# Optimization experiments

Measured on AMD Instinct MI355X. Metric: run time of the kernel, lower is better.

The kernel has to match this reference:

```python
import jax, jax.numpy as jnp
import numpy as np
from math import sqrt

B, L, S, H, E, D = 2, 2048, 2048, 16, 64, 64

def setup_inputs() -> dict:
    key = jax.random.key(0)
    kq, kk, kv = jax.random.split(key, 3)
    queries = jax.random.normal(kq, (B, L, H, E), dtype=jnp.float32)
    keys = jax.random.normal(kk, (B, S, H, E), dtype=jnp.float32)
    values = jax.random.normal(kv, (B, S, H, D), dtype=jnp.float32)
    # causal mask: True where attention is NOT allowed (j > i), matching masked_fill_ semantics
    causal = jnp.triu(jnp.ones((L, S), dtype=jnp.bool_), k=1)
    attn_mask = jnp.broadcast_to(causal[None, None, :, :], (B, 1, L, S))
    return {"queries": queries, "keys": keys, "values": values, "attn_mask": attn_mask}

def reference(queries, keys, values, attn_mask):
    # scores: [B,H,L,S]
    scale = 1.0 / sqrt(queries.shape[-1])
    scores = jnp.einsum('blhe,bshe->bhls', queries, keys)
    scores = jnp.where(attn_mask, -jnp.inf, scores)
    A = jax.nn.softmax(scale * scores, axis=-1)
    V = jnp.einsum('bhls,bshd->blhd', A, values)
    return V
```

## Files before the change

kernel.cpp:

```cpp
#include <hip/hip_runtime.h>

typedef unsigned short ushort_t;
typedef __attribute__((ext_vector_type(8))) short s8v;
typedef __attribute__((ext_vector_type(4))) short s4v;
typedef __attribute__((ext_vector_type(4))) float f4;

__device__ __forceinline__ ushort_t f2bf(float x) {
    unsigned u = __builtin_bit_cast(unsigned, x);
    return (ushort_t)((u + 0x7FFFu + ((u >> 16) & 1u)) >> 16);
}

__global__ __launch_bounds__(256) void prep_k(const float* __restrict__ K,
                                              ushort_t* __restrict__ Kb) {
    const int gid = blockIdx.x * 256 + threadIdx.x;
    const int e = (gid & 7) * 8;
    const int h = (gid >> 3) & 15;
    const int s = (gid >> 7) & 2047;
    const int b = gid >> 18;
    const float* src = K + (((b * 2048 + s) * 16 + h) * 64 + e);
    f4 a = *(const f4*)src;
    f4 c = *(const f4*)(src + 4);
    s8v o;
    #pragma unroll
    for (int j = 0; j < 4; ++j) { o[j] = (short)f2bf(a[j]); o[j + 4] = (short)f2bf(c[j]); }
    *(s8v*)(Kb + (((b * 16 + h) * 2048 + s) * 64 + e)) = o;
}

__global__ __launch_bounds__(256) void prep_v(const float* __restrict__ V,
                                              ushort_t* __restrict__ VT) {
    __shared__ ushort_t T[64 * 72];
    const int s0 = (blockIdx.x & 31) * 64;
    const int h  = (blockIdx.x >> 5) & 15;
    const int b  = blockIdx.x >> 9;
    const int t  = threadIdx.x;
    {
        const int srow = t >> 2, dc = (t & 3) * 16;
        const float* src = V + (((b * 2048 + s0 + srow) * 16 + h) * 64 + dc);
        #pragma unroll
        for (int c = 0; c < 4; ++c) {
            f4 v = *(const f4*)(src + c * 4);
            #pragma unroll
            for (int j = 0; j < 4; ++j) T[(dc + c * 4 + j) * 72 + srow] = f2bf(v[j]);
        }
    }
    __syncthreads();
    {
        const int d = t >> 2, sq = (t & 3) * 16;
        ushort_t* dst = VT + (((b * 16 + h) * 64 + d) * 2048 + s0 + sq);
        *(s8v*)(dst)     = *(const s8v*)(&T[d * 72 + sq]);
        *(s8v*)(dst + 8) = *(const s8v*)(&T[d * 72 + sq + 8]);
    }
}

__global__ __launch_bounds__(128, 2) void fattn_main(
    const float* __restrict__ Q,
    const ushort_t* __restrict__ Kb,
    const ushort_t* __restrict__ VTb,
    float* __restrict__ O)
{
    constexpr float K1 = 0.18033688011112042f;
    constexpr float SHIFT = 12.0f;
    __shared__ ushort_t P[2][4 * 640];
    __shared__ float Obuf[32 * 64];
    __shared__ float Lbuf[32];

    const int bx = blockIdx.x;
    const int bh = (bx & 7) | (((bx >> 3) & 3) << 3);
    const int pr = bx >> 5;
    const int b = bh >> 4, h = bh & 15;

    const int wave = threadIdx.x >> 6;
    const int lane = threadIdx.x & 63;
    const int l15  = lane & 15;
    const int quad = lane >> 4;

    const ushort_t* kb  = Kb  + bh * (2048 * 64);
    const ushort_t* vtb = VTb + bh * (64 * 2048);
    const float*    qb  = Q + b * (2048 * 1024) + h * 64;
    float*          ob  = O + b * (2048 * 1024) + h * 64;

    const s8v ones = {0x3F80, 0x3F80, 0x3F80, 0x3F80, 0x3F80, 0x3F80, 0x3F80, 0x3F80};
    const f4 zero4 = {0.f, 0.f, 0.f, 0.f};
    ushort_t* Pw = P[wave];

    for (int half = 0; half < 2; ++half) {
        const int i   = half ? (63 - pr) : pr;
        const int qr0 = i * 32;
        const int il  = i >> 1;

        s8v aq[2][2];
        #pragma unroll
        for (int m = 0; m < 2; ++m) {
            const float* qrow = qb + (qr0 + m * 16 + l15) * 1024;
            #pragma unroll
            for (int ks = 0; ks < 2; ++ks) {
                f4 x = *(const f4*)(qrow + ks * 32 + quad * 8);
                f4 y = *(const f4*)(qrow + ks * 32 + quad * 8 + 4);
                #pragma unroll
                for (int j = 0; j < 4; ++j) {
                    aq[m][ks][j]     = (short)f2bf(x[j]);
                    aq[m][ks][j + 4] = (short)f2bf(y[j]);
                }
            }
        }

        f4 oacc[2][4];
        f4 lsum[2] = {zero4, zero4};
        #pragma unroll
        for (int m = 0; m < 2; ++m)
            #pragma unroll
            for (int d = 0; d < 4; ++d) oacc[m][d] = zero4;

        for (int it = wave; it <= il; it += 2) {
            const int n0 = it * 64;
            const ushort_t* kp = kb + n0 * 64;
            const ushort_t* vp = vtb + n0;

            s8v bk[4][2];
            #pragma unroll
            for (int t = 0; t < 4; ++t)
                #pragma unroll
                for (int ks = 0; ks < 2; ++ks)
                    bk[t][ks] = *(const s8v*)(kp + (t * 16 + l15) * 64 + ks * 32 + quad * 8);
            s8v bv[4][2];
            #pragma unroll
            for (int dd = 0; dd < 4; ++dd)
                #pragma unroll
                for (int ks = 0; ks < 2; ++ks)
                    bv[dd][ks] = *(const s8v*)(vp + (dd * 16 + l15) * 2048 + ks * 32 + quad * 8);

            f4 sacc[2][4];
            #pragma unroll
            for (int m = 0; m < 2; ++m)
                #pragma unroll
                for (int t = 0; t < 4; ++t) {
                    f4 a = __builtin_amdgcn_mfma_f32_16x16x32_bf16(aq[m][0], bk[t][0], zero4, 0, 0, 0);
                    sacc[m][t] = __builtin_amdgcn_mfma_f32_16x16x32_bf16(aq[m][1], bk[t][1], a, 0, 0, 0);
                }

            const bool diag = (it == il);
            #pragma unroll
            for (int m = 0; m < 2; ++m)
                #pragma unroll
                for (int t = 0; t < 4; ++t)
                    #pragma unroll
                    for (int r = 0; r < 4; ++r) {
                        float x = __builtin_fmaf(sacc[m][t][r], K1, -SHIFT);
                        if (diag) {
                            const int gi = qr0 + m * 16 + quad * 4 + r;
                            const int gj = n0 + t * 16 + l15;
                            if (gj > gi) x = -INFINITY;
                        }
                        const float p = __builtin_exp2f(x);
                        const unsigned pb = __builtin_bit_cast(unsigned, p);
                        Pw[t * 640 + (m * 16 + quad * 4 + r) * 20 + l15] = (ushort_t)(pb >> 16);
                    }

            #pragma unroll
            for (int m = 0; m < 2; ++m)
                #pragma unroll
                for (int ks = 0; ks < 2; ++ks) {
                    const ushort_t* pp = Pw + (ks * 2 + (quad >> 1)) * 640
                                            + (m * 16 + l15) * 20 + (quad & 1) * 8;
                    s4v p0 = *(const s4v*)(pp);
                    s4v p1 = *(const s4v*)(pp + 4);
                    s8v ap = __builtin_shufflevector(p0, p1, 0, 1, 2, 3, 4, 5, 6, 7);
                    lsum[m] = __builtin_amdgcn_mfma_f32_16x16x32_bf16(ap, ones, lsum[m], 0, 0, 0);
                    #pragma unroll
                    for (int dd = 0; dd < 4; ++dd)
                        oacc[m][dd] = __builtin_amdgcn_mfma_f32_16x16x32_bf16(ap, bv[dd][ks], oacc[m][dd], 0, 0, 0);
                }
        }

        __syncthreads();
        if (wave == 1) {
            #pragma unroll
            for (int m = 0; m < 2; ++m) {
                #pragma unroll
                for (int dd = 0; dd < 4; ++dd)
                    #pragma unroll
                    for (int r = 0; r < 4; ++r)
                        Obuf[(m * 16 + quad * 4 + r) * 64 + dd * 16 + l15] = oacc[m][dd][r];
                if (l15 == 0)
                    #pragma unroll
                    for (int r = 0; r < 4; ++r) Lbuf[m * 16 + quad * 4 + r] = lsum[m][r];
            }
        }
        __syncthreads();
        if (wave == 0) {
            #pragma unroll
            for (int m = 0; m < 2; ++m)
                #pragma unroll
                for (int r = 0; r < 4; ++r) {
                    const int row = m * 16 + quad * 4 + r;
                    const float inv = 1.0f / (lsum[m][r] + Lbuf[row]);
                    #pragma unroll
                    for (int dd = 0; dd < 4; ++dd)
                        ob[(qr0 + row) * 1024 + dd * 16 + l15] =
                            (oacc[m][dd][r] + Obuf[row * 64 + dd * 16 + l15]) * inv;
                }
        }
    }
}

#define PSTR 72
__global__ __launch_bounds__(256) void fattn_fallback(
    const float* __restrict__ Q, const float* __restrict__ K,
    const float* __restrict__ V, float* __restrict__ O)
{
    constexpr int strL = 1024, strB = 2048 * strL;
    const float scale = 0.125f;
    __shared__ ushort_t KT[64 * PSTR];
    __shared__ ushort_t VT[64 * PSTR];
    __shared__ ushort_t P[4][16 * PSTR];
    const int bh = blockIdx.x & 31;
    const int b = bh >> 4, h = bh & 15;
    const int im = 31 - (blockIdx.x >> 5);
    const int q0 = im * 64;
    const int tid = threadIdx.x, wave = tid >> 6, lane = tid & 63;
    const int l15 = lane & 15, quad = lane >> 4;
    const float* qbase = Q + b*strB + (q0 + wave*16 + l15)*strL + h*64;
    s8v aq0, aq1;
    {
        f4 q0v = *(const f4*)(qbase + quad*8);
        f4 q1v = *(const f4*)(qbase + quad*8 + 4);
        f4 q2v = *(const f4*)(qbase + 32 + quad*8);
        f4 q3v = *(const f4*)(qbase + 32 + quad*8 + 4);
        #pragma unroll
        for (int j = 0; j < 4; ++j) {
            aq0[j] = (short)f2bf(q0v[j]); aq0[j+4] = (short)f2bf(q1v[j]);
            aq1[j] = (short)f2bf(q2v[j]); aq1[j+4] = (short)f2bf(q3v[j]);
        }
    }
    const f4 zero4 = {0.f,0.f,0.f,0.f};
    f4 oacc[4]; float m_prev[4], lsum[4];
    #pragma unroll
    for (int d = 0; d < 4; ++d) oacc[d] = zero4;
    #pragma unroll
    for (int r = 0; r < 4; ++r) { m_prev[r] = -INFINITY; lsum[r] = 0.0f; }
    const float* kh = K + b*strB + h*64;
    const float* vh = V + b*strB + h*64;
    for (int it = 0; it <= im; ++it) {
        const int n0 = it * 64;
        __syncthreads();
        {
            const float* krow = kh + (n0 + lane)*strL + wave*16;
            f4 k0 = *(const f4*)(krow); f4 k1 = *(const f4*)(krow+4);
            f4 k2 = *(const f4*)(krow+8); f4 k3 = *(const f4*)(krow+12);
            s8v kb0, kb1;
            #pragma unroll
            for (int j = 0; j < 4; ++j) {
                kb0[j] = (short)f2bf(k0[j]); kb0[j+4] = (short)f2bf(k1[j]);
                kb1[j] = (short)f2bf(k2[j]); kb1[j+4] = (short)f2bf(k3[j]);
            }
            *(s8v*)&KT[lane*PSTR + wave*16] = kb0;
            *(s8v*)&KT[lane*PSTR + wave*16 + 8] = kb1;
            const float* vrow = vh + (n0 + lane)*strL + wave*16;
            f4 v0 = *(const f4*)(vrow); f4 v1 = *(const f4*)(vrow+4);
            f4 v2 = *(const f4*)(vrow+8); f4 v3 = *(const f4*)(vrow+12);
            #pragma unroll
            for (int j = 0; j < 4; ++j) {
                VT[(wave*16 + j)*PSTR + lane] = f2bf(v0[j]);
                VT[(wave*16 + 4 + j)*PSTR + lane] = f2bf(v1[j]);
                VT[(wave*16 + 8 + j)*PSTR + lane] = f2bf(v2[j]);
                VT[(wave*16 + 12 + j)*PSTR + lane] = f2bf(v3[j]);
            }
        }
        __syncthreads();
        f4 sacc[4];
        #pragma unroll
        for (int t = 0; t < 4; ++t) {
            sacc[t] = zero4;
            const s8v bk0 = *(const s8v*)&KT[(t*16 + l15)*PSTR + quad*8];
            const s8v bk1 = *(const s8v*)&KT[(t*16 + l15)*PSTR + 32 + quad*8];
            sacc[t] = __builtin_amdgcn_mfma_f32_16x16x32_bf16(aq0, bk0, sacc[t], 0, 0, 0);
            sacc[t] = __builtin_amdgcn_mfma_f32_16x16x32_bf16(aq1, bk1, sacc[t], 0, 0, 0);
        }
        const bool diag = (it == im);
        float sv[4][4], rmax[4];
        #pragma unroll
        for (int r = 0; r < 4; ++r) rmax[r] = -INFINITY;
        #pragma unroll
        for (int t = 0; t < 4; ++t)
            #pragma unroll
            for (int r = 0; r < 4; ++r) {
                float x = sacc[t][r] * scale;
                if (diag) {
                    const int gi = wave*16 + quad*4 + r;
                    const int gj = t*16 + l15;
                    if (gj > gi) x = -INFINITY;
                }
                sv[t][r] = x; rmax[r] = fmaxf(rmax[r], x);
            }
        #pragma unroll
        for (int off = 8; off >= 1; off >>= 1)
            #pragma unroll
            for (int r = 0; r < 4; ++r)
                rmax[r] = fmaxf(rmax[r], __shfl_xor(rmax[r], off, 64));
        float mnew[4], alpha[4], rsum[4];
        #pragma unroll
        for (int r = 0; r < 4; ++r) {
            mnew[r] = fmaxf(m_prev[r], rmax[r]);
            alpha[r] = __expf(m_prev[r] - mnew[r]);
            m_prev[r] = mnew[r]; rsum[r] = 0.f;
        }
        #pragma unroll
        for (int t = 0; t < 4; ++t)
            #pragma unroll
            for (int r = 0; r < 4; ++r) {
                const float p = __expf(sv[t][r] - mnew[r]);
                rsum[r] += p;
                P[wave][(quad*4 + r)*PSTR + t*16 + l15] = f2bf(p);
            }
        #pragma unroll
        for (int off = 8; off >= 1; off >>= 1)
            #pragma unroll
            for (int r = 0; r < 4; ++r)
                rsum[r] += __shfl_xor(rsum[r], off, 64);
        #pragma unroll
        for (int r = 0; r < 4; ++r) lsum[r] = alpha[r]*lsum[r] + rsum[r];
        #pragma unroll
        for (int d = 0; d < 4; ++d)
            #pragma unroll
            for (int r = 0; r < 4; ++r) oacc[d][r] *= alpha[r];
        #pragma unroll
        for (int ks = 0; ks < 2; ++ks) {
            const s8v ap = *(const s8v*)&P[wave][l15*PSTR + ks*32 + quad*8];
            #pragma unroll
            for (int d = 0; d < 4; ++d) {
                const s8v bvv = *(const s8v*)&VT[(d*16 + l15)*PSTR + ks*32 + quad*8];
                oacc[d] = __builtin_amdgcn_mfma_f32_16x16x32_bf16(ap, bvv, oacc[d], 0, 0, 0);
            }
        }
    }
    float* obase = O + b*strB + h*64;
    #pragma unroll
    for (int r = 0; r < 4; ++r) {
        const float inv = 1.0f / lsum[r];
        const int gi = q0 + wave*16 + quad*4 + r;
        #pragma unroll
        for (int d = 0; d < 4; ++d)
            obase[gi*strL + d*16 + l15] = oacc[d][r] * inv;
    }
}

extern "C" void kernel_launch(void* const* d_in, const int* in_sizes, int n_in,
                              void* d_out, int out_size, void* d_ws, size_t ws_size,
                              hipStream_t stream) {
    const float* Q = (const float*)d_in[0];
    const float* K = (const float*)d_in[1];
    const float* V = (const float*)d_in[2];
    float* O = (float*)d_out;
    const size_t NEED = 2ull * 4194304ull * 2ull;
    if (ws_size >= NEED) {
        ushort_t* Kb = (ushort_t*)d_ws;
        ushort_t* VT = Kb + 4194304;
        prep_k<<<2048, 256, 0, stream>>>(K, Kb);
        prep_v<<<1024, 256, 0, stream>>>(V, VT);
        fattn_main<<<1024, 128, 0, stream>>>(Q, Kb, VT, O);
    } else {
        fattn_fallback<<<1024, 256, 0, stream>>>(Q, K, V, O);
    }
}
```

Measured before the change: 172.2 us.

## Fuse K/V prep kernels, use four waves per block, transpose S tiles

Merges the K and V bf16 conversion kernels into one launch to drop a kernel launch gap. The attention kernel goes from 2 to 4 waves per block, splitting KV tiles across four waves and reducing their partial outputs serially through shared memory. QK^T is computed transposed so each lane packs its P values and writes them to LDS as one 8-byte store, then reads them back as contiguous 16-byte loads. The final output is written with vectorized float4 stores. In exchange, the serial 4-step reduction adds barriers and LDS traffic, and the larger blocks raise register and occupancy pressure.

```diff
diff --git a/kernel.cpp b/kernel.cpp
--- a/kernel.cpp
+++ b/kernel.cpp
@@ -2,57 +2,64 @@
 
 typedef unsigned short ushort_t;
 typedef __attribute__((ext_vector_type(8))) short s8v;
-typedef __attribute__((ext_vector_type(4))) short s4v;
+typedef __attribute__((ext_vector_type(2))) unsigned u2v;
 typedef __attribute__((ext_vector_type(4))) float f4;
 
 __device__ __forceinline__ ushort_t f2bf(float x) {
     unsigned u = __builtin_bit_cast(unsigned, x);
     return (ushort_t)((u + 0x7FFFu + ((u >> 16) & 1u)) >> 16);
 }
-
-__global__ __launch_bounds__(256) void prep_k(const float* __restrict__ K,
-                                              ushort_t* __restrict__ Kb) {
-    const int gid = blockIdx.x * 256 + threadIdx.x;
-    const int e = (gid & 7) * 8;
-    const int h = (gid >> 3) & 15;
-    const int s = (gid >> 7) & 2047;
-    const int b = gid >> 18;
-    const float* src = K + (((b * 2048 + s) * 16 + h) * 64 + e);
-    f4 a = *(const f4*)src;
-    f4 c = *(const f4*)(src + 4);
-    s8v o;
-    #pragma unroll
-    for (int j = 0; j < 4; ++j) { o[j] = (short)f2bf(a[j]); o[j + 4] = (short)f2bf(c[j]); }
-    *(s8v*)(Kb + (((b * 16 + h) * 2048 + s) * 64 + e)) = o;
-}
-
-__global__ __launch_bounds__(256) void prep_v(const float* __restrict__ V,
-                                              ushort_t* __restrict__ VT) {
+__device__ __forceinline__ unsigned pack_hi16(float lo, float hi) {
+    unsigned a = __builtin_bit_cast(unsigned, lo);
+    unsigned b = __builtin_bit_cast(unsigned, hi);
+    return (a >> 16) | (b & 0xFFFF0000u);
+}
+
+__global__ __launch_bounds__(256) void prep_kv(const float* __restrict__ K,
+                                               const float* __restrict__ V,
+                                               ushort_t* __restrict__ Kb,
+                                               ushort_t* __restrict__ VT) {
     __shared__ ushort_t T[64 * 72];
-    const int s0 = (blockIdx.x & 31) * 64;
-    const int h  = (blockIdx.x >> 5) & 15;
-    const int b  = blockIdx.x >> 9;
-    const int t  = threadIdx.x;
-    {
-        const int srow = t >> 2, dc = (t & 3) * 16;
-        const float* src = V + (((b * 2048 + s0 + srow) * 16 + h) * 64 + dc);
-        #pragma unroll
-        for (int c = 0; c < 4; ++c) {
-            f4 v = *(const f4*)(src + c * 4);
-            #pragma unroll
-            for (int j = 0; j < 4; ++j) T[(dc + c * 4 + j) * 72 + srow] = f2bf(v[j]);
-        }
-    }
-    __syncthreads();
-    {
-        const int d = t >> 2, sq = (t & 3) * 16;
-        ushort_t* dst = VT + (((b * 16 + h) * 64 + d) * 2048 + s0 + sq);
-        *(s8v*)(dst)     = *(const s8v*)(&T[d * 72 + sq]);
-        *(s8v*)(dst + 8) = *(const s8v*)(&T[d * 72 + sq + 8]);
-    }
-}
-
-__global__ __launch_bounds__(128, 2) void fattn_main(
+    if (blockIdx.x < 2048) {
+        const int gid = blockIdx.x * 256 + threadIdx.x;
+        const int e = (gid & 7) * 8;
+        const int h = (gid >> 3) & 15;
+        const int s = (gid >> 7) & 2047;
+        const int b = gid >> 18;
+        const float* src = K + (((b * 2048 + s) * 16 + h) * 64 + e);
+        f4 a = *(const f4*)src;
+        f4 c = *(const f4*)(src + 4);
+        s8v o;
+        #pragma unroll
+        for (int j = 0; j < 4; ++j) { o[j] = (short)f2bf(a[j]); o[j + 4] = (short)f2bf(c[j]); }
+        *(s8v*)(Kb + (((b * 16 + h) * 2048 + s) * 64 + e)) = o;
+    } else {
+        const int v = blockIdx.x - 2048;
+        const int s0 = (v & 31) * 64;
+        const int h  = (v >> 5) & 15;
+        const int b  = v >> 9;
+        const int t  = threadIdx.x;
+        {
+            const int srow = t >> 2, dc = (t & 3) * 16;
+            const float* src = V + (((b * 2048 + s0 + srow) * 16 + h) * 64 + dc);
+            #pragma unroll
+            for (int c = 0; c < 4; ++c) {
+                f4 vv = *(const f4*)(src + c * 4);
+                #pragma unroll
+                for (int j = 0; j < 4; ++j) T[(dc + c * 4 + j) * 72 + srow] = f2bf(vv[j]);
+            }
+        }
+        __syncthreads();
+        {
+            const int d = t >> 2, sq = (t & 3) * 16;
+            ushort_t* dst = VT + (((b * 16 + h) * 64 + d) * 2048 + s0 + sq);
+            *(s8v*)(dst)     = *(const s8v*)(&T[d * 72 + sq]);
+            *(s8v*)(dst + 8) = *(const s8v*)(&T[d * 72 + sq + 8]);
+        }
+    }
+}
+
+__global__ __launch_bounds__(256, 4) void fattn_main(
     const float* __restrict__ Q,
     const ushort_t* __restrict__ Kb,
     const ushort_t* __restrict__ VTb,
@@ -60,12 +67,12 @@
 {
     constexpr float K1 = 0.18033688011112042f;
     constexpr float SHIFT = 12.0f;
-    __shared__ ushort_t P[2][4 * 640];
+    __shared__ ushort_t P[8][16 * 72];
     __shared__ float Obuf[32 * 64];
     __shared__ float Lbuf[32];
 
     const int bx = blockIdx.x;
-    const int bh = (bx & 7) | (((bx >> 3) & 3) << 3);
+    const int bh = bx & 31;
     const int pr = bx >> 5;
     const int b = bh >> 4, h = bh & 15;
 
@@ -81,7 +88,6 @@
 
     const s8v ones = {0x3F80, 0x3F80, 0x3F80, 0x3F80, 0x3F80, 0x3F80, 0x3F80, 0x3F80};
     const f4 zero4 = {0.f, 0.f, 0.f, 0.f};
-    ushort_t* Pw = P[wave];
 
     for (int half = 0; half < 2; ++half) {
         const int i   = half ? (63 - pr) : pr;
@@ -111,7 +117,7 @@
             #pragma unroll
             for (int d = 0; d < 4; ++d) oacc[m][d] = zero4;
 
-        for (int it = wave; it <= il; it += 2) {
+        for (int it = wave; it <= il; it += 4) {
             const int n0 = it * 64;
             const ushort_t* kp = kb + n0 * 64;
             const ushort_t* vp = vtb + n0;
@@ -129,76 +135,83 @@
                 for (int ks = 0; ks < 2; ++ks)
                     bv[dd][ks] = *(const s8v*)(vp + (dd * 16 + l15) * 2048 + ks * 32 + quad * 8);
 
-            f4 sacc[2][4];
-            #pragma unroll
-            for (int m = 0; m < 2; ++m)
+            const bool diag = (it == il);
+
+            #pragma unroll
+            for (int m = 0; m < 2; ++m) {
+                ushort_t* Pm = P[wave * 2 + m];
                 #pragma unroll
                 for (int t = 0; t < 4; ++t) {
-                    f4 a = __builtin_amdgcn_mfma_f32_16x16x32_bf16(aq[m][0], bk[t][0], zero4, 0, 0, 0);
-                    sacc[m][t] = __builtin_amdgcn_mfma_f32_16x16x32_bf16(aq[m][1], bk[t][1], a, 0, 0, 0);
-                }
-
-            const bool diag = (it == il);
-            #pragma unroll
-            for (int m = 0; m < 2; ++m)
-                #pragma unroll
-                for (int t = 0; t < 4; ++t)
+                    f4 a  = __builtin_amdgcn_mfma_f32_16x16x32_bf16(bk[t][0], aq[m][0], zero4, 0, 0, 0);
+                    f4 st = __builtin_amdgcn_mfma_f32_16x16x32_bf16(bk[t][1], aq[m][1], a, 0, 0, 0);
+                    float p[4];
                     #pragma unroll
                     for (int r = 0; r < 4; ++r) {
-                        float x = __builtin_fmaf(sacc[m][t][r], K1, -SHIFT);
+                        float x = __builtin_fmaf(st[r], K1, -SHIFT);
                         if (diag) {
-                            const int gi = qr0 + m * 16 + quad * 4 + r;
-                            const int gj = n0 + t * 16 + l15;
+                            const int gj = n0 + t * 16 + quad * 4 + r;
+                            const int gi = qr0 + m * 16 + l15;
                             if (gj > gi) x = -INFINITY;
                         }
-                        const float p = __builtin_exp2f(x);
-                        const unsigned pb = __builtin_bit_cast(unsigned, p);
-                        Pw[t * 640 + (m * 16 + quad * 4 + r) * 20 + l15] = (ushort_t)(pb >> 16);
+                        p[r] = __builtin_exp2f(x);
                     }
-
-            #pragma unroll
-            for (int m = 0; m < 2; ++m)
+                    u2v pk;
+                    pk[0] = pack_hi16(p[0], p[1]);
+                    pk[1] = pack_hi16(p[2], p[3]);
+                    *(u2v*)&Pm[l15 * 72 + t * 16 + quad * 4] = pk;
+                }
+            }
+
+            #pragma unroll
+            for (int m = 0; m < 2; ++m) {
+                const ushort_t* Pm = P[wave * 2 + m];
                 #pragma unroll
                 for (int ks = 0; ks < 2; ++ks) {
-                    const ushort_t* pp = Pw + (ks * 2 + (quad >> 1)) * 640
-                                            + (m * 16 + l15) * 20 + (quad & 1) * 8;
-                    s4v p0 = *(const s4v*)(pp);
-                    s4v p1 = *(const s4v*)(pp + 4);
-                    s8v ap = __builtin_shufflevector(p0, p1, 0, 1, 2, 3, 4, 5, 6, 7);
+                    const s8v ap = *(const s8v*)&Pm[l15 * 72 + ks * 32 + quad * 8];
                     lsum[m] = __builtin_amdgcn_mfma_f32_16x16x32_bf16(ap, ones, lsum[m], 0, 0, 0);
                     #pragma unroll
                     for (int dd = 0; dd < 4; ++dd)
                         oacc[m][dd] = __builtin_amdgcn_mfma_f32_16x16x32_bf16(ap, bv[dd][ks], oacc[m][dd], 0, 0, 0);
                 }
+            }
         }
 
         __syncthreads();
-        if (wave == 1) {
-            #pragma unroll
-            for (int m = 0; m < 2; ++m) {
-                #pragma unroll
-                for (int dd = 0; dd < 4; ++dd)
-                    #pragma unroll
-                    for (int r = 0; r < 4; ++r)
-                        Obuf[(m * 16 + quad * 4 + r) * 64 + dd * 16 + l15] = oacc[m][dd][r];
-                if (l15 == 0)
-                    #pragma unroll
-                    for (int r = 0; r < 4; ++r) Lbuf[m * 16 + quad * 4 + r] = lsum[m][r];
-            }
-        }
-        __syncthreads();
-        if (wave == 0) {
-            #pragma unroll
-            for (int m = 0; m < 2; ++m)
-                #pragma unroll
-                for (int r = 0; r < 4; ++r) {
-                    const int row = m * 16 + quad * 4 + r;
-                    const float inv = 1.0f / (lsum[m][r] + Lbuf[row]);
+        #pragma unroll
+        for (int w = 0; w < 4; ++w) {
+            if (wave == w) {
+                #pragma unroll
+                for (int m = 0; m < 2; ++m) {
                     #pragma unroll
                     for (int dd = 0; dd < 4; ++dd)
-                        ob[(qr0 + row) * 1024 + dd * 16 + l15] =
-                            (oacc[m][dd][r] + Obuf[row * 64 + dd * 16 + l15]) * inv;
-                }
+                        #pragma unroll
+                        for (int r = 0; r < 4; ++r) {
+                            const int idx = (m * 16 + quad * 4 + r) * 64 + dd * 16 + l15;
+                            if (w == 0) Obuf[idx] = oacc[m][dd][r];
+                            else        Obuf[idx] += oacc[m][dd][r];
+                        }
+                    if (l15 == 0)
+                        #pragma unroll
+                        for (int r = 0; r < 4; ++r) {
+                            const int row = m * 16 + quad * 4 + r;
+                            if (w == 0) Lbuf[row] = lsum[m][r];
+                            else        Lbuf[row] += lsum[m][r];
+                        }
+                }
+            }
+            __syncthreads();
+        }
+        {
+            const int row = wave * 8 + (lane >> 3);
+            const int c0  = (lane & 7) * 8;
+            const float inv = 1.0f / Lbuf[row];
+            f4 o0 = *(const f4*)&Obuf[row * 64 + c0];
+            f4 o1 = *(const f4*)&Obuf[row * 64 + c0 + 4];
+            #pragma unroll
+            for (int j = 0; j < 4; ++j) { o0[j] *= inv; o1[j] *= inv; }
+            float* dst = ob + (qr0 + row) * 1024 + c0;
+            *(f4*)dst       = o0;
+            *(f4*)(dst + 4) = o1;
         }
     }
 }
@@ -355,9 +368,8 @@
     if (ws_size >= NEED) {
         ushort_t* Kb = (ushort_t*)d_ws;
         ushort_t* VT = Kb + 4194304;
-        prep_k<<<2048, 256, 0, stream>>>(K, Kb);
-        prep_v<<<1024, 256, 0, stream>>>(V, VT);
-        fattn_main<<<1024, 128, 0, stream>>>(Q, Kb, VT, O);
+        prep_kv<<<3072, 256, 0, stream>>>(K, V, Kb, VT);
+        fattn_main<<<1024, 256, 0, stream>>>(Q, Kb, VT, O);
     } else {
         fattn_fallback<<<1024, 256, 0, stream>>>(Q, K, V, O);
     }
```

New measurement: 183.7 us. +6.7%, slower.
